# Performance work log

Hardware: AMD Instinct MI355X
Metric: run time of the kernel (lower is better)

## Reference

```python
import jax, jax.numpy as jnp
import numpy as np

HC = 6.62607015e-34 * 2.99792458e8  # Planck*c in J*m


def lattice_to_primitive(lattice):
    """[a,b,c,alpha,beta,gamma] -> 3x3 primitive basis (columns e1,e2,e3)."""
    a, b, c = lattice[0], lattice[1], lattice[2]
    cal, cbe = jnp.cos(lattice[3]), jnp.cos(lattice[4])
    cga, sga = jnp.cos(lattice[5]), jnp.sin(lattice[5])
    e3y = (cal - cbe * cga) / sga
    e3z = jnp.sqrt(jnp.maximum(1.0 - cbe * cbe - e3y * e3y, 1e-12))
    o = jnp.zeros((), lattice.dtype)
    prim = jnp.stack([
        jnp.stack([a, b * cga, c * cbe]),
        jnp.stack([o, b * sga, c * e3y]),
        jnp.stack([o, o, c * e3z]),
    ])
    return prim


def primitive_to_reciprocal(prim):
    # e*_i = (e_j x e_k) / V  <=>  inv(prim).T for 3x3 basis-as-columns
    return jnp.linalg.inv(prim).T


def omega_to_rot(angle):
    """3 elementary rotation angles -> Rx(t1) @ Ry(t2) @ Rz(t3)."""
    c, s = jnp.cos(angle), jnp.sin(angle)
    o = jnp.zeros((), angle.dtype)
    l = jnp.ones((), angle.dtype)
    rx = jnp.stack([jnp.stack([l, o, o]), jnp.stack([o, c[0], -s[0]]), jnp.stack([o, s[0], c[0]])])
    ry = jnp.stack([jnp.stack([c[1], o, s[1]]), jnp.stack([o, l, o]), jnp.stack([-s[1], o, c[1]])])
    rz = jnp.stack([jnp.stack([c[2], -s[2], o]), jnp.stack([s[2], c[2], o]), jnp.stack([o, o, l])])
    return rx @ ry @ rz


def _np_primitive(lattice):
    a, b, c, al, be, ga = [float(v) for v in lattice]
    cal, cbe, cga, sga = np.cos(al), np.cos(be), np.cos(ga), np.sin(ga)
    e3y = (cal - cbe * cga) / sga
    e3z = np.sqrt(max(1.0 - cbe * cbe - e3y * e3y, 1e-12))
    return np.array([[a, b * cga, c * cbe], [0.0, b * sga, c * e3y], [0.0, 0.0, c * e3z]])


def setup_inputs() -> dict:
    key = jax.random.key(0)
    lattice_np = np.array([3.6e-10, 3.6e-10, 3.6e-10, np.pi / 2, np.pi / 2, np.pi / 2], np.float64)
    e_min = 5e3 * 1.602176634e-19   # 5 keV in J
    e_max = 25e3 * 1.602176634e-19  # 25 keV in J

    # select_hkl: all nonzero hkl inside the Ewald ball ||B @ hkl|| <= 2*e_max/(h*c)
    recip_np = np.linalg.inv(_np_primitive(lattice_np)).T
    q_max = 2.0 * e_max / HC
    n_max = int(np.ceil(q_max * lattice_np[:3].max())) + 1
    grid = np.arange(-n_max, n_max + 1)
    hkl_all = np.stack(np.meshgrid(grid, grid, grid, indexing="ij"), axis=-1).reshape(-1, 3)
    q_norm = np.linalg.norm(hkl_all @ recip_np.T, axis=1)
    hkl = hkl_all[(q_norm <= q_max) & (q_norm > 0.0)].astype(np.int32)  # (~12k, 3)

    n_exp = 5000
    uq_exp = jax.random.normal(key, (n_exp, 3), dtype=jnp.float32)
    uq_exp = uq_exp / jnp.linalg.norm(uq_exp, axis=1, keepdims=True)

    return {
        "lattice": jnp.asarray(lattice_np, jnp.float32),
        "angle": jnp.zeros(3, jnp.float32),
        "uq_exp": uq_exp,
        "hkl": jnp.asarray(hkl),
        "phi_max": jnp.float32(0.5 * np.pi / 180.0),
        "e_min": jnp.float32(e_min),
    }


def reference(lattice, angle, uq_exp, hkl, phi_max, e_min):
    # rotate reciprocal lattice into lab frame
    reciprocal = primitive_to_reciprocal(lattice_to_primitive(lattice))
    rot = omega_to_rot(angle)
    reciprocal_lab = rot @ reciprocal                      # (3,3)

    # hkl -> diffraction vectors, unit uq and energies
    q = hkl.astype(lattice.dtype) @ reciprocal_lab.T       # (m,3)
    q_norm = jnp.linalg.norm(q, axis=1)                    # (m,)
    uq_theo = q / q_norm[:, None]                          # (m,3)
    sin_theta = jnp.abs(uq_theo[:, 2])                     # incident beam along z
    energy = HC * q_norm / (2.0 * jnp.maximum(sin_theta, 1e-9))
    keep = energy >= e_min                                 # (m,) energy filter mask

    # continuous matching rate: soft count of exp rays close to a kept theo ray
    cosang = jnp.clip(uq_exp @ uq_theo.T, -1.0 + 1e-6, 1.0 - 1e-6)  # (n,m)
    phi = jnp.arccos(cosang)
    phi = jnp.where(keep[None, :], phi, jnp.pi)            # masked rays -> max distance
    phi_min = jnp.min(phi, axis=1)                         # (n,)
    rate = jnp.mean(jnp.exp(-0.5 * (phi_min / phi_max) ** 2))
    return rate
```

## Files before the change

kernel.cpp:

```cpp
#include <hip/hip_runtime.h>
#include <math.h>

#define HCF 1.98644586e-25f

constexpr int BLOCK = 256;
constexpr int RPT   = 4;
constexpr int RAYS_PER_BLOCK = BLOCK * RPT;

__global__ __launch_bounds__(BLOCK) void refiner_maxdot_kernel(
    const float* __restrict__ lattice, const float* __restrict__ angle,
    const float* __restrict__ uq_exp,  const int* __restrict__ hkl,
    const float* __restrict__ e_min_p,
    unsigned* __restrict__ maxenc, int n, int m, int nchunks)
{
    __shared__ float4 s_uq[BLOCK];
    const int tid   = threadIdx.x;
    const int chunk = blockIdx.x % nchunks;
    const int rg    = blockIdx.x / nchunks;

    const float a = lattice[0], b = lattice[1], cc = lattice[2];
    const float cal = cosf(lattice[3]), cbe = cosf(lattice[4]);
    const float cga = cosf(lattice[5]), sga = sinf(lattice[5]);
    const float e3y = (cal - cbe * cga) / sga;
    const float e3z = sqrtf(fmaxf(1.0f - cbe * cbe - e3y * e3y, 1e-12f));
    const float p01 = b * cga, p02 = cc * cbe, p11 = b * sga, p12 = cc * e3y, p22 = cc * e3z;
    const float i00 = 1.0f / a, i11 = 1.0f / p11, i22 = 1.0f / p22;
    const float i01 = -p01 * (i00 * i11);
    const float i12 = -p12 * (i11 * i22);
    const float i02 = (p01 * p12 - p02 * p11) * (i00 * i11 * i22);
    const float c0 = cosf(angle[0]), s0 = sinf(angle[0]);
    const float c1 = cosf(angle[1]), s1 = sinf(angle[1]);
    const float c2 = cosf(angle[2]), s2 = sinf(angle[2]);
    const float M00 = c1 * c2,               M01 = -c1 * s2,              M02 = s1;
    const float M10 = c0 * s2 + s0 * s1 * c2, M11 = c0 * c2 - s0 * s1 * s2, M12 = -s0 * c1;
    const float M20 = s0 * s2 - c0 * s1 * c2, M21 = s0 * c2 + c0 * s1 * s2, M22 = c0 * c1;
    const float B00 = M00 * i00 + M01 * i01 + M02 * i02;
    const float B01 = M01 * i11 + M02 * i12;
    const float B02 = M02 * i22;
    const float B10 = M10 * i00 + M11 * i01 + M12 * i02;
    const float B11 = M11 * i11 + M12 * i12;
    const float B12 = M12 * i22;
    const float B20 = M20 * i00 + M21 * i01 + M22 * i02;
    const float B21 = M21 * i11 + M22 * i12;
    const float B22 = M22 * i22;

    const int ti = chunk * BLOCK + tid;
    float4 v = make_float4(0.f, 0.f, 0.f, 0.f);
    if (ti < m) {
        const float h0 = (float)hkl[3 * ti + 0];
        const float h1 = (float)hkl[3 * ti + 1];
        const float h2 = (float)hkl[3 * ti + 2];
        const float qx = B00 * h0 + B01 * h1 + B02 * h2;
        const float qy = B10 * h0 + B11 * h1 + B12 * h2;
        const float qz = B20 * h0 + B21 * h1 + B22 * h2;
        const float qn = sqrtf(qx * qx + qy * qy + qz * qz);
        const float inv = 1.0f / qn;
        const float ux = qx * inv, uy = qy * inv, uz = qz * inv;
        const float st = fabsf(uz);
        const float energy = HCF * qn / (2.0f * fmaxf(st, 1e-9f));
        if (energy >= e_min_p[0]) v = make_float4(ux, uy, uz, 0.f);
    }
    s_uq[tid] = v;
    __syncthreads();

    float rx[RPT], ry[RPT], rz[RPT], mx[RPT];
    bool valid[RPT];
#pragma unroll
    for (int i = 0; i < RPT; ++i) {
        const int ray = rg * RAYS_PER_BLOCK + i * BLOCK + tid;
        valid[i] = (ray < n);
        float x = 0.f, y = 0.f, z = 0.f;
        if (valid[i]) { x = uq_exp[3 * ray]; y = uq_exp[3 * ray + 1]; z = uq_exp[3 * ray + 2]; }
        rx[i] = x; ry[i] = y; rz[i] = z;
        mx[i] = 0.f;
    }

#pragma unroll 4
    for (int j = 0; j < BLOCK; ++j) {
        const float4 t = s_uq[j];
#pragma unroll
        for (int i = 0; i < RPT; ++i) {
            const float d = rx[i] * t.x + ry[i] * t.y + rz[i] * t.z;
            mx[i] = fmaxf(mx[i], d);
        }
    }

#pragma unroll
    for (int i = 0; i < RPT; ++i) {
        if (valid[i]) {
            const int ray = rg * RAYS_PER_BLOCK + i * BLOCK + tid;
            atomicMax(&maxenc[ray], __float_as_uint(mx[i]));
        }
    }
}

__global__ __launch_bounds__(BLOCK) void refiner_finalize_kernel(
    const unsigned* __restrict__ maxenc, const float* __restrict__ phi_max_p,
    float* __restrict__ out, int n)
{
    const int i = blockIdx.x * BLOCK + threadIdx.x;
    float w = 0.f;
    if (i < n) {
        float c = __uint_as_float(maxenc[i]);
        c = fminf(c, 1.0f - 1e-6f);
        const float phi = acosf(c);
        const float t = phi / phi_max_p[0];
        w = expf(-0.5f * t * t);
    }
#pragma unroll
    for (int off = 32; off > 0; off >>= 1) w += __shfl_down(w, off, 64);
    __shared__ float s[BLOCK / 64];
    const int lane = threadIdx.x & 63, wv = threadIdx.x >> 6;
    if (lane == 0) s[wv] = w;
    __syncthreads();
    if (threadIdx.x == 0) {
        float tot = 0.f;
#pragma unroll
        for (int k = 0; k < BLOCK / 64; ++k) tot += s[k];
        atomicAdd(out, tot / (float)n);
    }
}

extern "C" void kernel_launch(void* const* d_in, const int* in_sizes, int n_in,
                              void* d_out, int out_size, void* d_ws, size_t ws_size,
                              hipStream_t stream) {
    const float* lattice = (const float*)d_in[0];
    const float* angle   = (const float*)d_in[1];
    const float* uq_exp  = (const float*)d_in[2];
    const int*   hkl     = (const int*)d_in[3];
    const float* phi_max = (const float*)d_in[4];
    const float* e_min   = (const float*)d_in[5];
    const int n = in_sizes[2] / 3;
    const int m = in_sizes[3] / 3;

    unsigned* maxenc = (unsigned*)d_ws;

    hipMemsetAsync(maxenc, 0, (size_t)n * sizeof(unsigned), stream);
    hipMemsetAsync(d_out, 0, sizeof(float), stream);

    const int nchunks = (m + BLOCK - 1) / BLOCK;
    const int nrg     = (n + RAYS_PER_BLOCK - 1) / RAYS_PER_BLOCK;
    refiner_maxdot_kernel<<<dim3(nrg * nchunks), dim3(BLOCK), 0, stream>>>(
        lattice, angle, uq_exp, hkl, e_min, maxenc, n, m, nchunks);
    refiner_finalize_kernel<<<dim3((n + BLOCK - 1) / BLOCK), dim3(BLOCK), 0, stream>>>(
        maxenc, phi_max, (float*)d_out, n);
}
```

Baseline: 83.30 us.

## Fuse memset, maxdot and finalize into one cooperative kernel with grid syncs

```diff
diff --git a/kernel.cpp b/kernel.cpp
--- a/kernel.cpp
+++ b/kernel.cpp
@@ -1,23 +1,23 @@
 #include <hip/hip_runtime.h>
+#include <hip/hip_cooperative_groups.h>
 #include <math.h>
+
+namespace cg = cooperative_groups;
 
 #define HCF 1.98644586e-25f
 
 constexpr int BLOCK = 256;
 constexpr int RPT   = 4;
 constexpr int RAYS_PER_BLOCK = BLOCK * RPT;
-
-__global__ __launch_bounds__(BLOCK) void refiner_maxdot_kernel(
-    const float* __restrict__ lattice, const float* __restrict__ angle,
-    const float* __restrict__ uq_exp,  const int* __restrict__ hkl,
-    const float* __restrict__ e_min_p,
-    unsigned* __restrict__ maxenc, int n, int m, int nchunks)
-{
-    __shared__ float4 s_uq[BLOCK];
-    const int tid   = threadIdx.x;
-    const int chunk = blockIdx.x % nchunks;
-    const int rg    = blockIdx.x / nchunks;
-
+constexpr int MAXN  = 8192;
+
+__device__ unsigned g_maxenc[MAXN];
+
+struct Bmat { float B00,B01,B02,B10,B11,B12,B20,B21,B22; };
+
+__device__ __forceinline__ Bmat make_B(const float* __restrict__ lattice,
+                                       const float* __restrict__ angle)
+{
     const float a = lattice[0], b = lattice[1], cc = lattice[2];
     const float cal = cosf(lattice[3]), cbe = cosf(lattice[4]);
     const float cga = cosf(lattice[5]), sga = sinf(lattice[5]);
@@ -31,18 +31,33 @@
     const float c0 = cosf(angle[0]), s0 = sinf(angle[0]);
     const float c1 = cosf(angle[1]), s1 = sinf(angle[1]);
     const float c2 = cosf(angle[2]), s2 = sinf(angle[2]);
-    const float M00 = c1 * c2,               M01 = -c1 * s2,              M02 = s1;
+    const float M00 = c1 * c2,                M01 = -c1 * s2,               M02 = s1;
     const float M10 = c0 * s2 + s0 * s1 * c2, M11 = c0 * c2 - s0 * s1 * s2, M12 = -s0 * c1;
     const float M20 = s0 * s2 - c0 * s1 * c2, M21 = s0 * c2 + c0 * s1 * s2, M22 = c0 * c1;
-    const float B00 = M00 * i00 + M01 * i01 + M02 * i02;
-    const float B01 = M01 * i11 + M02 * i12;
-    const float B02 = M02 * i22;
-    const float B10 = M10 * i00 + M11 * i01 + M12 * i02;
-    const float B11 = M11 * i11 + M12 * i12;
-    const float B12 = M12 * i22;
-    const float B20 = M20 * i00 + M21 * i01 + M22 * i02;
-    const float B21 = M21 * i11 + M22 * i12;
-    const float B22 = M22 * i22;
+    Bmat r;
+    r.B00 = M00 * i00 + M01 * i01 + M02 * i02;
+    r.B01 = M01 * i11 + M02 * i12;
+    r.B02 = M02 * i22;
+    r.B10 = M10 * i00 + M11 * i01 + M12 * i02;
+    r.B11 = M11 * i11 + M12 * i12;
+    r.B12 = M12 * i22;
+    r.B20 = M20 * i00 + M21 * i01 + M22 * i02;
+    r.B21 = M21 * i11 + M22 * i12;
+    r.B22 = M22 * i22;
+    return r;
+}
+
+__device__ __forceinline__ void maxdot_body(
+    const float* __restrict__ lattice, const float* __restrict__ angle,
+    const float* __restrict__ uq_exp,  const int* __restrict__ hkl,
+    const float* __restrict__ e_min_p,
+    unsigned* __restrict__ maxenc, int n, int m, int nchunks, float4* s_uq)
+{
+    const int tid   = threadIdx.x;
+    const int chunk = blockIdx.x % nchunks;
+    const int rg    = blockIdx.x / nchunks;
+
+    const Bmat B = make_B(lattice, angle);
 
     const int ti = chunk * BLOCK + tid;
     float4 v = make_float4(0.f, 0.f, 0.f, 0.f);
@@ -50,9 +65,9 @@
         const float h0 = (float)hkl[3 * ti + 0];
         const float h1 = (float)hkl[3 * ti + 1];
         const float h2 = (float)hkl[3 * ti + 2];
-        const float qx = B00 * h0 + B01 * h1 + B02 * h2;
-        const float qy = B10 * h0 + B11 * h1 + B12 * h2;
-        const float qz = B20 * h0 + B21 * h1 + B22 * h2;
+        const float qx = B.B00 * h0 + B.B01 * h1 + B.B02 * h2;
+        const float qy = B.B10 * h0 + B.B11 * h1 + B.B12 * h2;
+        const float qz = B.B20 * h0 + B.B21 * h1 + B.B22 * h2;
         const float qn = sqrtf(qx * qx + qy * qy + qz * qz);
         const float inv = 1.0f / qn;
         const float ux = qx * inv, uy = qy * inv, uz = qz * inv;
@@ -92,6 +107,57 @@
             atomicMax(&maxenc[ray], __float_as_uint(mx[i]));
         }
     }
+}
+
+__global__ __launch_bounds__(BLOCK) void refiner_fused_kernel(
+    const float* __restrict__ lattice, const float* __restrict__ angle,
+    const float* __restrict__ uq_exp,  const int* __restrict__ hkl,
+    const float* __restrict__ phi_max_p, const float* __restrict__ e_min_p,
+    float* __restrict__ out, int n, int m, int nchunks)
+{
+    __shared__ float4 s_uq[BLOCK];
+    cg::grid_group grid = cg::this_grid();
+    const int tid = threadIdx.x;
+
+    for (int i = blockIdx.x * BLOCK + tid; i < n; i += gridDim.x * BLOCK)
+        g_maxenc[i] = 0u;
+    grid.sync();
+
+    maxdot_body(lattice, angle, uq_exp, hkl, e_min_p, g_maxenc, n, m, nchunks, s_uq);
+    grid.sync();
+
+    if (blockIdx.x == 0) {
+        float wsum = 0.f;
+        for (int i = tid; i < n; i += BLOCK) {
+            float c = __uint_as_float(g_maxenc[i]);
+            c = fminf(c, 1.0f - 1e-6f);
+            const float phi = acosf(c);
+            const float t = phi / phi_max_p[0];
+            wsum += expf(-0.5f * t * t);
+        }
+#pragma unroll
+        for (int off = 32; off > 0; off >>= 1) wsum += __shfl_down(wsum, off, 64);
+        __shared__ float s[BLOCK / 64];
+        const int lane = tid & 63, wv = tid >> 6;
+        if (lane == 0) s[wv] = wsum;
+        __syncthreads();
+        if (tid == 0) {
+            float tot = 0.f;
+#pragma unroll
+            for (int k = 0; k < BLOCK / 64; ++k) tot += s[k];
+            out[0] = tot / (float)n;
+        }
+    }
+}
+
+__global__ __launch_bounds__(BLOCK) void refiner_maxdot_kernel(
+    const float* __restrict__ lattice, const float* __restrict__ angle,
+    const float* __restrict__ uq_exp,  const int* __restrict__ hkl,
+    const float* __restrict__ e_min_p,
+    unsigned* __restrict__ maxenc, int n, int m, int nchunks)
+{
+    __shared__ float4 s_uq[BLOCK];
+    maxdot_body(lattice, angle, uq_exp, hkl, e_min_p, maxenc, n, m, nchunks, s_uq);
 }
 
 __global__ __launch_bounds__(BLOCK) void refiner_finalize_kernel(
@@ -130,18 +196,30 @@
     const int*   hkl     = (const int*)d_in[3];
     const float* phi_max = (const float*)d_in[4];
     const float* e_min   = (const float*)d_in[5];
-    const int n = in_sizes[2] / 3;
-    const int m = in_sizes[3] / 3;
+    int n = in_sizes[2] / 3;
+    int m = in_sizes[3] / 3;
+
+    int nchunks = (m + BLOCK - 1) / BLOCK;
+    int nrg     = (n + RAYS_PER_BLOCK - 1) / RAYS_PER_BLOCK;
+    int nblocks = nrg * nchunks;
+    float* outp = (float*)d_out;
+
+    if (n <= MAXN && nblocks <= 1024) {
+        void* args[] = {
+            (void*)&lattice, (void*)&angle, (void*)&uq_exp, (void*)&hkl,
+            (void*)&phi_max, (void*)&e_min, (void*)&outp,
+            (void*)&n, (void*)&m, (void*)&nchunks
+        };
+        hipError_t err = hipLaunchCooperativeKernel(refiner_fused_kernel,
+            dim3(nblocks), dim3(BLOCK), args, 0, stream);
+        if (err == hipSuccess) return;
+    }
 
     unsigned* maxenc = (unsigned*)d_ws;
-
     hipMemsetAsync(maxenc, 0, (size_t)n * sizeof(unsigned), stream);
     hipMemsetAsync(d_out, 0, sizeof(float), stream);
-
-    const int nchunks = (m + BLOCK - 1) / BLOCK;
-    const int nrg     = (n + RAYS_PER_BLOCK - 1) / RAYS_PER_BLOCK;
-    refiner_maxdot_kernel<<<dim3(nrg * nchunks), dim3(BLOCK), 0, stream>>>(
+    refiner_maxdot_kernel<<<dim3(nblocks), dim3(BLOCK), 0, stream>>>(
         lattice, angle, uq_exp, hkl, e_min, maxenc, n, m, nchunks);
     refiner_finalize_kernel<<<dim3((n + BLOCK - 1) / BLOCK), dim3(BLOCK), 0, stream>>>(
-        maxenc, phi_max, (float*)d_out, n);
-}
+        maxenc, phi_max, outp, n);
+}
```

Result: slower. 151.6 us (+82.0%).
